# Performance work log

Hardware: AMD Instinct MI355X
Metric: run time of the kernel (lower is better)

The kernel has to match this reference:

```python
import jax, jax.numpy as jnp
import numpy as np

# dims
B = 4096; BEGIN = 0; END = 2048; N_OBJ = 64; D_OBJ = 32
PI_IN = 31; PI_H = 256; EMB = 256; H = 4; HD = 64; OTH_IN = 256; OTH_H = 256; OTH_OUT = 256

def _lin_init(k, fan_in, fan_out):
    b = np.sqrt(6.0 / (fan_in + fan_out))
    return jax.random.uniform(k, (fan_in, fan_out), jnp.float32, -b, b)

def setup_inputs() -> dict:
    key = jax.random.key(0)
    ks = jax.random.split(key, 8)
    obs = jax.random.normal(ks[0], (B, BEGIN + (END - BEGIN) + OTH_IN), jnp.float32)
    inp = {
        "obs": obs,
        # others encoder MLP: 256 -> 256 -> 256
        "oW1": _lin_init(ks[1], OTH_IN, OTH_H), "ob1": jnp.zeros((OTH_H,), jnp.float32),
        "oW2": _lin_init(ks[2], OTH_H, OTH_OUT), "ob2": jnp.zeros((OTH_OUT,), jnp.float32),
        # per-object pi MLP: 31 -> 256 -> 256 -> 256
        "pW1": _lin_init(ks[3], PI_IN, PI_H), "pb1": jnp.zeros((PI_H,), jnp.float32),
        "pW2": _lin_init(ks[4], PI_H, PI_H), "pb2": jnp.zeros((PI_H,), jnp.float32),
        "pW3": _lin_init(ks[5], PI_H, EMB), "pb3": jnp.zeros((EMB,), jnp.float32),
        # attention projections
        "Wq": _lin_init(ks[6], OTH_OUT, H * HD), "bq": jnp.zeros((H * HD,), jnp.float32),
        # per-head K/V projections (MultiHeadProj): [H, HD, HD], stored as x @ W per head
        "Wk": jax.random.uniform(jax.random.fold_in(key, 10), (H, HD, HD), jnp.float32, -np.sqrt(6.0/(2*HD)), np.sqrt(6.0/(2*HD))),
        "bk": jnp.zeros((H, HD), jnp.float32),
        "Wv": jax.random.uniform(jax.random.fold_in(key, 11), (H, HD, HD), jnp.float32, -np.sqrt(6.0/(2*HD)), np.sqrt(6.0/(2*HD))),
        "bv": jnp.zeros((H, HD), jnp.float32),
    }
    return inp

def reference(obs, oW1, ob1, oW2, ob2, pW1, pb1, pW2, pb2, pW3, pb3, Wq, bq, Wk, bk, Wv, bv):
    # split obs
    objs = obs[:, BEGIN:END].reshape(-1, N_OBJ, D_OBJ)
    others = jnp.concatenate([obs[:, :BEGIN], obs[:, END:]], axis=1)
    # others encoder
    others_e = jax.nn.relu(others @ oW1 + ob1) @ oW2 + ob2           # [B, 256]
    # mask + per-object MLP
    mask = objs[:, :, -1]                                            # [B, N]
    feats = objs[:, :, :-1]                                          # [B, N, 31]
    h = jax.nn.relu(feats @ pW1 + pb1)
    h = jax.nn.relu(h @ pW2 + pb2)
    emb = (h @ pW3 + pb3) * mask[:, :, None]                         # [B, N, EMB]
    # attention
    q = (others_e @ Wq + bq).reshape(-1, H, 1, HD)                   # [B, H, 1, HD]
    e = emb.reshape(-1, N_OBJ, H, HD)                                # [B, N, H, HD]
    key = jnp.einsum('bnhd,hde->bnhe', e, Wk) + bk                   # per-head linear
    val = (jnp.einsum('bnhd,hde->bnhe', e, Wv) + bv) * mask[:, :, None, None]
    logits = jnp.einsum('bhqd,bnhd->bhqn', q, key) / np.sqrt(EMB)    # [B, H, 1, N]
    logits = jnp.where(mask[:, None, None, :] == 0, -1e9, logits)
    attn = jax.nn.softmax(logits, axis=-1)
    out_emb = jnp.einsum('bhqn,bnhd->bhqd', attn, val).reshape(-1, EMB)
    return jnp.concatenate([others_e, out_emb], axis=1)             # [B, 512]
```

## Files before the change

### kernel.cpp

```cpp
#include <hip/hip_runtime.h>

#define BATCH      4096
#define OBS_COLS   2304
#define OTH_OFF    2048
#define EMB        256
#define OUTC       512

#define QK_BYTES   (4096u * 256u * 4u)
#define QB_BYTES   (4096u * 4u * 4u)

typedef __bf16 bf16x8 __attribute__((ext_vector_type(8)));
typedef __bf16 bf16x4 __attribute__((ext_vector_type(4)));
typedef float  f32x16 __attribute__((ext_vector_type(16)));

#define S_PW1  0
#define S_PW2  2
#define S_PW3  18
#define N_SLICE 34

__device__ __forceinline__ int shx(int row, int col) {
    return (row << 8) + ((((col >> 3) ^ (row & 31)) << 3) | (col & 7));
}

__global__ __launch_bounds__(512, 2) void k_oth(
    const float* __restrict__ obs,
    const float* __restrict__ oW1, const float* __restrict__ ob1,
    const float* __restrict__ oW2, const float* __restrict__ ob2,
    const float* __restrict__ Wq,  const float* __restrict__ bq,
    const float* __restrict__ Wk,  const float* __restrict__ bk,
    const float* __restrict__ pW1, const float* __restrict__ pW2,
    const float* __restrict__ pW3,
    float* __restrict__ out, float* __restrict__ qkg,
    float* __restrict__ qbg, __bf16* __restrict__ wp)
{
    __shared__ __align__(16) __bf16 s_a[32 * 256];
    __shared__ __align__(16) __bf16 s_h[32 * 256];
    __shared__ __align__(16) __bf16 s_q[32 * 256];
    __shared__ float s_qb[32 * 4];

    const int t  = threadIdx.x;
    const int b0 = blockIdx.x * 32;
    const int wv = t >> 6, lane = t & 63;
    const int lm = lane & 31, lh = lane >> 5;
    const int ct = wv;

    if (blockIdx.x < N_SLICE) {
        const int s = blockIdx.x;
        int kt; const float* W; int isW1 = 0;
        if      (s < S_PW2) { kt = s;         W = pW1; isW1 = 1; }
        else if (s < S_PW3) { kt = s - S_PW2; W = pW2; }
        else                { kt = s - S_PW3; W = pW3; }
        const int kbase = kt * 16 + lh * 8;
        const int n     = (t >> 6) * 32 + lm;
        bf16x8 v;
        #pragma unroll
        for (int j = 0; j < 8; ++j) {
            const int k = kbase + j;
            const float f = (isW1 && k >= 31) ? 0.0f : W[k * 256 + n];
            v[j] = (__bf16)f;
        }
        ((bf16x8*)wp)[(size_t)s * 512 + t] = v;
    }

    #pragma unroll
    for (int i = 0; i < 2; ++i) {
        const int c = i * 512 + t;
        const int row = c >> 5, seg = c & 31;
        const float* src = obs + (size_t)(b0 + row) * OBS_COLS + OTH_OFF + seg * 8;
        const float4 v0 = ((const float4*)src)[0];
        const float4 v1 = ((const float4*)src)[1];
        bf16x8 o;
        o[0]=(__bf16)v0.x; o[1]=(__bf16)v0.y; o[2]=(__bf16)v0.z; o[3]=(__bf16)v0.w;
        o[4]=(__bf16)v1.x; o[5]=(__bf16)v1.y; o[6]=(__bf16)v1.z; o[7]=(__bf16)v1.w;
        *(bf16x8*)&s_a[shx(row, seg * 8)] = o;
    }
    if (t < 128) s_qb[t] = 0.0f;
    __syncthreads();

    f32x16 acc;
    f32x16 vzero;
    #pragma unroll
    for (int i = 0; i < 16; ++i) vzero[i] = 0.0f;

    {
        const float* Wl = oW1 + (size_t)(lh * 8) * 256 + ct * 32 + lm;
        acc = vzero;
        float f[8];
        #pragma unroll
        for (int j = 0; j < 8; ++j) f[j] = Wl[j * 256];
        #pragma unroll 4
        for (int kt = 0; kt < 16; ++kt) {
            float fn[8];
            const int kn = (kt + 1) & 15;
            #pragma unroll
            for (int j = 0; j < 8; ++j) fn[j] = Wl[(kn * 16 + j) * 256];
            bf16x8 b;
            #pragma unroll
            for (int j = 0; j < 8; ++j) b[j] = (__bf16)f[j];
            const bf16x8 a = *(const bf16x8*)&s_a[shx(lm, kt * 16 + lh * 8)];
            acc = __builtin_amdgcn_mfma_f32_32x32x16_bf16(b, a, acc, 0, 0, 0);
            #pragma unroll
            for (int j = 0; j < 8; ++j) f[j] = fn[j];
        }
        const float* bias = &ob1[ct * 32 + 4 * lh];
        #pragma unroll
        for (int g = 0; g < 4; ++g) {
            bf16x4 v;
            #pragma unroll
            for (int q = 0; q < 4; ++q)
                v[q] = (__bf16)fmaxf(acc[g * 4 + q] + bias[8 * g + q], 0.0f);
            *(bf16x4*)&s_h[(lm << 8) + ((((ct << 2) + g) ^ lm) << 3) + 4 * lh] = v;
        }
    }
    __syncthreads();

    {
        const float* Wl = oW2 + (size_t)(lh * 8) * 256 + ct * 32 + lm;
        acc = vzero;
        float f[8];
        #pragma unroll
        for (int j = 0; j < 8; ++j) f[j] = Wl[j * 256];
        #pragma unroll 4
        for (int kt = 0; kt < 16; ++kt) {
            float fn[8];
            const int kn = (kt + 1) & 15;
            #pragma unroll
            for (int j = 0; j < 8; ++j) fn[j] = Wl[(kn * 16 + j) * 256];
            bf16x8 b;
            #pragma unroll
            for (int j = 0; j < 8; ++j) b[j] = (__bf16)f[j];
            const bf16x8 a = *(const bf16x8*)&s_h[shx(lm, kt * 16 + lh * 8)];
            acc = __builtin_amdgcn_mfma_f32_32x32x16_bf16(b, a, acc, 0, 0, 0);
            #pragma unroll
            for (int j = 0; j < 8; ++j) f[j] = fn[j];
        }
        const float* bias = &ob2[ct * 32 + 4 * lh];
        float* dstg = &out[(size_t)(b0 + lm) * OUTC + ct * 32 + 4 * lh];
        #pragma unroll
        for (int g = 0; g < 4; ++g) {
            float4 fv; bf16x4 v;
            float* fp = &fv.x;
            #pragma unroll
            for (int q = 0; q < 4; ++q) {
                const float f2 = acc[g * 4 + q] + bias[8 * g + q];
                fp[q] = f2; v[q] = (__bf16)f2;
            }
            *(float4*)&dstg[8 * g] = fv;
            *(bf16x4*)&s_a[(lm << 8) + ((((ct << 2) + g) ^ lm) << 3) + 4 * lh] = v;
        }
    }
    __syncthreads();

    {
        const float* Wl = Wq + (size_t)(lh * 8) * 256 + ct * 32 + lm;
        acc = vzero;
        float f[8];
        #pragma unroll
        for (int j = 0; j < 8; ++j) f[j] = Wl[j * 256];
        #pragma unroll 4
        for (int kt = 0; kt < 16; ++kt) {
            float fn[8];
            const int kn = (kt + 1) & 15;
            #pragma unroll
            for (int j = 0; j < 8; ++j) fn[j] = Wl[(kn * 16 + j) * 256];
            bf16x8 b;
            #pragma unroll
            for (int j = 0; j < 8; ++j) b[j] = (__bf16)f[j];
            const bf16x8 a = *(const bf16x8*)&s_a[shx(lm, kt * 16 + lh * 8)];
            acc = __builtin_amdgcn_mfma_f32_32x32x16_bf16(b, a, acc, 0, 0, 0);
            #pragma unroll
            for (int j = 0; j < 8; ++j) f[j] = fn[j];
        }
        const int hh = ct >> 1;
        const float* bias = &bq[ct * 32 + 4 * lh];
        const float* bkp  = &bk[ct * 32 + 4 * lh];
        float part = 0.0f;
        #pragma unroll
        for (int g = 0; g < 4; ++g) {
            bf16x4 v;
            #pragma unroll
            for (int q = 0; q < 4; ++q) {
                const float f2 = acc[g * 4 + q] + bias[8 * g + q];
                part += f2 * bkp[8 * g + q];
                v[q] = (__bf16)f2;
            }
            *(bf16x4*)&s_q[(lm << 8) + ((((ct << 2) + g) ^ lm) << 3) + 4 * lh] = v;
        }
        part += __shfl_xor(part, 32, 64);
        if (lane < 32) atomicAdd(&s_qb[lm * 4 + hh], part);
    }
    __syncthreads();

    if (t < 128) qbg[(size_t)(b0 + (t >> 2)) * 4 + (t & 3)] = s_qb[t];

    {
        const int h = wv >> 1, c2 = wv & 1;
        acc = vzero;
        #pragma unroll
        for (int kt = 0; kt < 4; ++kt) {
            const float* wk = Wk + ((size_t)(h * 64 + c2 * 32 + lm) * 64 + kt * 16 + lh * 8);
            const float4 w0 = *(const float4*)wk;
            const float4 w1 = *(const float4*)(wk + 4);
            bf16x8 b;
            b[0]=(__bf16)w0.x; b[1]=(__bf16)w0.y; b[2]=(__bf16)w0.z; b[3]=(__bf16)w0.w;
            b[4]=(__bf16)w1.x; b[5]=(__bf16)w1.y; b[6]=(__bf16)w1.z; b[7]=(__bf16)w1.w;
            const bf16x8 a = *(const bf16x8*)&s_q[shx(lm, h * 64 + kt * 16 + lh * 8)];
            acc = __builtin_amdgcn_mfma_f32_32x32x16_bf16(b, a, acc, 0, 0, 0);
        }
        float* dstg = &qkg[(size_t)(b0 + lm) * 256 + h * 64 + c2 * 32 + 4 * lh];
        #pragma unroll
        for (int g = 0; g < 4; ++g) {
            float4 fv;
            float* fp = &fv.x;
            #pragma unroll
            for (int q = 0; q < 4; ++q) fp[q] = acc[g * 4 + q];
            *(float4*)&dstg[8 * g] = fv;
        }
    }
}

__global__ __launch_bounds__(512, 4) void k_obj(
    const float* __restrict__ obs,  const __bf16* __restrict__ wp,
    const float* __restrict__ pb1,  const float* __restrict__ pb2,
    const float* __restrict__ pb3,  const float* __restrict__ qkg,
    const float* __restrict__ qbg,  const float* __restrict__ bv,
    const float* __restrict__ Wv,   float* __restrict__ out)
{
    __shared__ __align__(16) __bf16 s_h[128 * 256];
    __shared__ __align__(16) char s_fp[128 * 40 * 2];
    __bf16* s_f = (__bf16*)s_fp;
    float*  s_p = (float*)s_fp;
    __shared__ float s_mask[128];
    __shared__ float s_qk[8 * 64];
    __shared__ float s_am[8 * 64];
    __shared__ float s_amsum[8];

    const int t  = threadIdx.x;
    const int b0 = blockIdx.x * 2;
    const int wv = t >> 6, lane = t & 63;
    const int lm = lane & 31, lh = lane >> 5;
    const int rtp = wv & 1;
    const int ct0 = (wv >> 1) * 2;
    const int row0 = rtp * 64 + lm;
    const int row1 = row0 + 32;

    bf16x8 b1[2][2];
    {
        const bf16x8* Bg = (const bf16x8*)wp + S_PW1 * 512;
        #pragma unroll
        for (int kt = 0; kt < 2; ++kt)
            #pragma unroll
            for (int c = 0; c < 2; ++c)
                b1[kt][c] = Bg[(kt * 8 + ct0 + c) * 64 + lane];
    }

    {
        const int row = t >> 2, q4 = t & 3;
        const float* src = obs + (size_t)(b0 + (row >> 6)) * OBS_COLS
                               + (row & 63) * 32 + q4 * 8;
        const float4 v0 = ((const float4*)src)[0];
        const float4 v1 = ((const float4*)src)[1];
        bf16x8 o;
        o[0]=(__bf16)v0.x; o[1]=(__bf16)v0.y; o[2]=(__bf16)v0.z; o[3]=(__bf16)v0.w;
        o[4]=(__bf16)v1.x; o[5]=(__bf16)v1.y; o[6]=(__bf16)v1.z; o[7]=(__bf16)v1.w;
        *(bf16x8*)&s_f[row * 40 + q4 * 8] = o;
        if (q4 == 3) s_mask[row] = v1.w;
    }
    if (t < 128) ((float4*)s_qk)[t] = ((const float4*)(qkg + (size_t)b0 * 256))[t];
    __syncthreads();

    f32x16 acc[2][2];
    f32x16 vzero;
    #pragma unroll
    for (int i = 0; i < 16; ++i) vzero[i] = 0.0f;

    {
        #pragma unroll
        for (int r = 0; r < 2; ++r)
            #pragma unroll
            for (int c = 0; c < 2; ++c) acc[r][c] = vzero;
        #pragma unroll
        for (int kt = 0; kt < 2; ++kt) {
            const bf16x8 a0 = *(const bf16x8*)&s_f[row0 * 40 + kt * 16 + lh * 8];
            const bf16x8 a1 = *(const bf16x8*)&s_f[row1 * 40 + kt * 16 + lh * 8];
            acc[0][0] = __builtin_amdgcn_mfma_f32_32x32x16_bf16(b1[kt][0], a0, acc[0][0], 0, 0, 0);
            acc[0][1] = __builtin_amdgcn_mfma_f32_32x32x16_bf16(b1[kt][1], a0, acc[0][1], 0, 0, 0);
            acc[1][0] = __builtin_amdgcn_mfma_f32_32x32x16_bf16(b1[kt][0], a1, acc[1][0], 0, 0, 0);
            acc[1][1] = __builtin_amdgcn_mfma_f32_32x32x16_bf16(b1[kt][1], a1, acc[1][1], 0, 0, 0);
        }
        #pragma unroll
        for (int r = 0; r < 2; ++r) {
            const int row = r ? row1 : row0;
            #pragma unroll
            for (int c = 0; c < 2; ++c) {
                const float* bias = &pb1[(ct0 + c) * 32 + 4 * lh];
                #pragma unroll
                for (int g = 0; g < 4; ++g) {
                    bf16x4 v;
                    #pragma unroll
                    for (int q = 0; q < 4; ++q)
                        v[q] = (__bf16)fmaxf(acc[r][c][g * 4 + q] + bias[8 * g + q], 0.0f);
                    *(bf16x4*)&s_h[(row << 8) + (((((ct0 + c) << 2) + g) ^ lm) << 3) + 4 * lh] = v;
                }
            }
        }
    }
    __syncthreads();

    {
        const bf16x8* Bg = (const bf16x8*)wp + S_PW2 * 512;
        #pragma unroll
        for (int r = 0; r < 2; ++r)
            #pragma unroll
            for (int c = 0; c < 2; ++c) acc[r][c] = vzero;
        bf16x8 bc0 = Bg[(ct0 + 0) * 64 + lane];
        bf16x8 bc1 = Bg[(ct0 + 1) * 64 + lane];
        #pragma unroll 4
        for (int kt = 0; kt < 16; ++kt) {
            const int kn = (kt + 1) & 15;
            const bf16x8 bn0 = Bg[(kn * 8 + ct0 + 0) * 64 + lane];
            const bf16x8 bn1 = Bg[(kn * 8 + ct0 + 1) * 64 + lane];
            const bf16x8 a0 = *(const bf16x8*)&s_h[(row0 << 8) + (((2 * kt + lh) ^ lm) << 3)];
            const bf16x8 a1 = *(const bf16x8*)&s_h[(row1 << 8) + (((2 * kt + lh) ^ lm) << 3)];
            acc[0][0] = __builtin_amdgcn_mfma_f32_32x32x16_bf16(bc0, a0, acc[0][0], 0, 0, 0);
            acc[0][1] = __builtin_amdgcn_mfma_f32_32x32x16_bf16(bc1, a0, acc[0][1], 0, 0, 0);
            acc[1][0] = __builtin_amdgcn_mfma_f32_32x32x16_bf16(bc0, a1, acc[1][0], 0, 0, 0);
            acc[1][1] = __builtin_amdgcn_mfma_f32_32x32x16_bf16(bc1, a1, acc[1][1], 0, 0, 0);
            bc0 = bn0; bc1 = bn1;
        }
        __syncthreads();
        #pragma unroll
        for (int r = 0; r < 2; ++r) {
            const int row = r ? row1 : row0;
            #pragma unroll
            for (int c = 0; c < 2; ++c) {
                const float* bias = &pb2[(ct0 + c) * 32 + 4 * lh];
                #pragma unroll
                for (int g = 0; g < 4; ++g) {
                    bf16x4 v;
                    #pragma unroll
                    for (int q = 0; q < 4; ++q)
                        v[q] = (__bf16)fmaxf(acc[r][c][g * 4 + q] + bias[8 * g + q], 0.0f);
                    *(bf16x4*)&s_h[(row << 8) + (((((ct0 + c) << 2) + g) ^ lm) << 3) + 4 * lh] = v;
                }
            }
        }
    }
    __syncthreads();

    {
        const bf16x8* Bg = (const bf16x8*)wp + S_PW3 * 512;
        #pragma unroll
        for (int r = 0; r < 2; ++r)
            #pragma unroll
            for (int c = 0; c < 2; ++c) acc[r][c] = vzero;
        bf16x8 bc0 = Bg[(ct0 + 0) * 64 + lane];
        bf16x8 bc1 = Bg[(ct0 + 1) * 64 + lane];
        #pragma unroll 4
        for (int kt = 0; kt < 16; ++kt) {
            const int kn = (kt + 1) & 15;
            const bf16x8 bn0 = Bg[(kn * 8 + ct0 + 0) * 64 + lane];
            const bf16x8 bn1 = Bg[(kn * 8 + ct0 + 1) * 64 + lane];
            const bf16x8 a0 = *(const bf16x8*)&s_h[(row0 << 8) + (((2 * kt + lh) ^ lm) << 3)];
            const bf16x8 a1 = *(const bf16x8*)&s_h[(row1 << 8) + (((2 * kt + lh) ^ lm) << 3)];
            acc[0][0] = __builtin_amdgcn_mfma_f32_32x32x16_bf16(bc0, a0, acc[0][0], 0, 0, 0);
            acc[0][1] = __builtin_amdgcn_mfma_f32_32x32x16_bf16(bc1, a0, acc[0][1], 0, 0, 0);
            acc[1][0] = __builtin_amdgcn_mfma_f32_32x32x16_bf16(bc0, a1, acc[1][0], 0, 0, 0);
            acc[1][1] = __builtin_amdgcn_mfma_f32_32x32x16_bf16(bc1, a1, acc[1][1], 0, 0, 0);
            bc0 = bn0; bc1 = bn1;
        }
        __syncthreads();
        #pragma unroll
        for (int r = 0; r < 2; ++r) {
            const int row = r ? row1 : row0;
            const float mk = s_mask[row];
            #pragma unroll
            for (int c = 0; c < 2; ++c) {
                const float* bias = &pb3[(ct0 + c) * 32 + 4 * lh];
                #pragma unroll
                for (int g = 0; g < 4; ++g) {
                    bf16x4 v;
                    #pragma unroll
                    for (int q = 0; q < 4; ++q)
                        v[q] = (__bf16)((acc[r][c][g * 4 + q] + bias[8 * g + q]) * mk);
                    *(bf16x4*)&s_h[(row << 8) + (((((ct0 + c) << 2) + g) ^ lm) << 3) + 4 * lh] = v;
                }
            }
        }
    }
    __syncthreads();

    {
        const int r = wv >> 2, h = wv & 3;
        const float qb = qbg[(size_t)(b0 + r) * 4 + h];
        const int erow = r * 64 + lane;
        float dot = 0.0f;
        #pragma unroll
        for (int d8 = 0; d8 < 8; ++d8) {
            const bf16x8 ev = *(const bf16x8*)&s_h[(erow << 8) + ((((h << 3) + d8) ^ (erow & 31)) << 3)];
            const float* kv = &s_qk[(r * 4 + h) * 64 + d8 * 8];
            #pragma unroll
            for (int j = 0; j < 8; ++j) dot += (float)ev[j] * kv[j];
        }
        const float mk = s_mask[erow];
        float logit = (dot + qb) * 0.0625f;
        if (mk == 0.0f) logit = -1.0e9f;
        float m = logit;
        #pragma unroll
        for (int off = 32; off > 0; off >>= 1) m = fmaxf(m, __shfl_xor(m, off, 64));
        const float ex = __expf(logit - m);
        float ssum = ex;
        #pragma unroll
        for (int off = 32; off > 0; off >>= 1) ssum += __shfl_xor(ssum, off, 64);
        const float am = (ex / ssum) * mk;
        s_am[(r * 4 + h) * 64 + lane] = am;
        float ams = am;
        #pragma unroll
        for (int off = 32; off > 0; off >>= 1) ams += __shfl_xor(ams, off, 64);
        if (lane == 0) s_amsum[r * 4 + h] = ams;
    }
    __syncthreads();

    {
        const int r = t >> 8, h = (t >> 6) & 3, d = t & 63;
        const float* amr = &s_am[(r * 4 + h) * 64];
        const int blkbase = (h << 3) + (d >> 3);
        const int doff = d & 7;
        float a = 0.0f;
        #pragma unroll 16
        for (int n = 0; n < 64; ++n) {
            const int row = r * 64 + n;
            a += amr[n] * (float)s_h[(row << 8) + (((blkbase ^ (row & 31)) << 3) | doff)];
        }
        s_p[(r * 4 + h) * 64 + d] = a;
    }
    __syncthreads();

    {
        const int r = t >> 8, h = (t >> 6) & 3, e = t & 63;
        float a = s_amsum[r * 4 + h] * bv[h * 64 + e];
        const float* pr  = &s_p[(r * 4 + h) * 64];
        const float* wvp = Wv + (size_t)h * 64 * 64 + e;
        #pragma unroll 16
        for (int d = 0; d < 64; ++d)
            a += pr[d] * wvp[d * 64];
        out[(size_t)(b0 + r) * OUTC + EMB + h * 64 + e] = a;
    }
}

extern "C" void kernel_launch(void* const* d_in, const int* in_sizes, int n_in,
                              void* d_out, int out_size, void* d_ws, size_t ws_size,
                              hipStream_t stream)
{
    const float* obs = (const float*)d_in[0];
    const float* oW1 = (const float*)d_in[1];
    const float* ob1 = (const float*)d_in[2];
    const float* oW2 = (const float*)d_in[3];
    const float* ob2 = (const float*)d_in[4];
    const float* pW1 = (const float*)d_in[5];
    const float* pb1 = (const float*)d_in[6];
    const float* pW2 = (const float*)d_in[7];
    const float* pb2 = (const float*)d_in[8];
    const float* pW3 = (const float*)d_in[9];
    const float* pb3 = (const float*)d_in[10];
    const float* Wq  = (const float*)d_in[11];
    const float* bq  = (const float*)d_in[12];
    const float* Wk  = (const float*)d_in[13];
    const float* bk  = (const float*)d_in[14];
    const float* Wv  = (const float*)d_in[15];
    const float* bv  = (const float*)d_in[16];
    float*  out = (float*)d_out;
    float*  qkg = (float*)d_ws;
    float*  qbg = (float*)((char*)d_ws + QK_BYTES);
    __bf16* wp  = (__bf16*)((char*)d_ws + QK_BYTES + QB_BYTES);

    k_oth<<<BATCH / 32, 512, 0, stream>>>(obs, oW1, ob1, oW2, ob2, Wq, bq,
                                          Wk, bk, pW1, pW2, pW3,
                                          out, qkg, qbg, wp);
    k_obj<<<BATCH / 2, 512, 0, stream>>>(obs, wp, pb1, pb2, pb3, qkg, qbg,
                                         bv, Wv, out);
}
```

Measured before the change: 229.6 us.

## Process one batch row per block and vectorize attention epilogue with shuffle reductions

After: 240.7 us. +4.8%, slower.

```diff
diff --git a/kernel.cpp b/kernel.cpp
--- a/kernel.cpp
+++ b/kernel.cpp
@@ -219,30 +219,30 @@
     }
 }
 
-__global__ __launch_bounds__(512, 4) void k_obj(
+__global__ __launch_bounds__(256, 4) void k_obj(
     const float* __restrict__ obs,  const __bf16* __restrict__ wp,
     const float* __restrict__ pb1,  const float* __restrict__ pb2,
     const float* __restrict__ pb3,  const float* __restrict__ qkg,
     const float* __restrict__ qbg,  const float* __restrict__ bv,
     const float* __restrict__ Wv,   float* __restrict__ out)
 {
-    __shared__ __align__(16) __bf16 s_h[128 * 256];
-    __shared__ __align__(16) char s_fp[128 * 40 * 2];
+    __shared__ __align__(16) __bf16 s_h[64 * 256];
+    __shared__ __align__(16) char s_fp[64 * 32 * 2];
     __bf16* s_f = (__bf16*)s_fp;
     float*  s_p = (float*)s_fp;
-    __shared__ float s_mask[128];
-    __shared__ float s_qk[8 * 64];
-    __shared__ float s_am[8 * 64];
-    __shared__ float s_amsum[8];
+    __shared__ float s_mask[64];
+    __shared__ float s_qk[4 * 64];
+    __shared__ float s_am[4 * 64];
+    __shared__ float s_amsum[4];
+    __shared__ float s_qb[4];
 
     const int t  = threadIdx.x;
-    const int b0 = blockIdx.x * 2;
+    const int b  = blockIdx.x;
     const int wv = t >> 6, lane = t & 63;
     const int lm = lane & 31, lh = lane >> 5;
-    const int rtp = wv & 1;
-    const int ct0 = (wv >> 1) * 2;
-    const int row0 = rtp * 64 + lm;
-    const int row1 = row0 + 32;
+    const int ct0 = wv * 2;
+    const int row0 = lm;
+    const int row1 = lm + 32;
 
     bf16x8 b1[2][2];
     {
@@ -256,17 +256,17 @@
 
     {
         const int row = t >> 2, q4 = t & 3;
-        const float* src = obs + (size_t)(b0 + (row >> 6)) * OBS_COLS
-                               + (row & 63) * 32 + q4 * 8;
+        const float* src = obs + (size_t)b * OBS_COLS + row * 32 + q4 * 8;
         const float4 v0 = ((const float4*)src)[0];
         const float4 v1 = ((const float4*)src)[1];
         bf16x8 o;
         o[0]=(__bf16)v0.x; o[1]=(__bf16)v0.y; o[2]=(__bf16)v0.z; o[3]=(__bf16)v0.w;
         o[4]=(__bf16)v1.x; o[5]=(__bf16)v1.y; o[6]=(__bf16)v1.z; o[7]=(__bf16)v1.w;
-        *(bf16x8*)&s_f[row * 40 + q4 * 8] = o;
+        *(bf16x8*)&s_f[row * 32 + q4 * 8] = o;
         if (q4 == 3) s_mask[row] = v1.w;
     }
-    if (t < 128) ((float4*)s_qk)[t] = ((const float4*)(qkg + (size_t)b0 * 256))[t];
+    if (t < 64) ((float4*)s_qk)[t] = ((const float4*)(qkg + (size_t)b * 256))[t];
+    if (t >= 64 && t < 68) s_qb[t - 64] = qbg[(size_t)b * 4 + (t - 64)];
     __syncthreads();
 
     f32x16 acc[2][2];
@@ -281,8 +281,8 @@
             for (int c = 0; c < 2; ++c) acc[r][c] = vzero;
         #pragma unroll
         for (int kt = 0; kt < 2; ++kt) {
-            const bf16x8 a0 = *(const bf16x8*)&s_f[row0 * 40 + kt * 16 + lh * 8];
-            const bf16x8 a1 = *(const bf16x8*)&s_f[row1 * 40 + kt * 16 + lh * 8];
+            const bf16x8 a0 = *(const bf16x8*)&s_f[row0 * 32 + kt * 16 + lh * 8];
+            const bf16x8 a1 = *(const bf16x8*)&s_f[row1 * 32 + kt * 16 + lh * 8];
             acc[0][0] = __builtin_amdgcn_mfma_f32_32x32x16_bf16(b1[kt][0], a0, acc[0][0], 0, 0, 0);
             acc[0][1] = __builtin_amdgcn_mfma_f32_32x32x16_bf16(b1[kt][1], a0, acc[0][1], 0, 0, 0);
             acc[1][0] = __builtin_amdgcn_mfma_f32_32x32x16_bf16(b1[kt][0], a1, acc[1][0], 0, 0, 0);
@@ -391,18 +391,17 @@
     __syncthreads();
 
     {
-        const int r = wv >> 2, h = wv & 3;
-        const float qb = qbg[(size_t)(b0 + r) * 4 + h];
-        const int erow = r * 64 + lane;
+        const int h = wv;
+        const float qb = s_qb[h];
         float dot = 0.0f;
         #pragma unroll
         for (int d8 = 0; d8 < 8; ++d8) {
-            const bf16x8 ev = *(const bf16x8*)&s_h[(erow << 8) + ((((h << 3) + d8) ^ (erow & 31)) << 3)];
-            const float* kv = &s_qk[(r * 4 + h) * 64 + d8 * 8];
+            const bf16x8 ev = *(const bf16x8*)&s_h[(lane << 8) + ((((h << 3) + d8) ^ (lane & 31)) << 3)];
+            const float* kv = &s_qk[h * 64 + d8 * 8];
             #pragma unroll
             for (int j = 0; j < 8; ++j) dot += (float)ev[j] * kv[j];
         }
-        const float mk = s_mask[erow];
+        const float mk = s_mask[lane];
         float logit = (dot + qb) * 0.0625f;
         if (mk == 0.0f) logit = -1.0e9f;
         float m = logit;
@@ -413,38 +412,75 @@
         #pragma unroll
         for (int off = 32; off > 0; off >>= 1) ssum += __shfl_xor(ssum, off, 64);
         const float am = (ex / ssum) * mk;
-        s_am[(r * 4 + h) * 64 + lane] = am;
+        s_am[h * 64 + lane] = am;
         float ams = am;
         #pragma unroll
         for (int off = 32; off > 0; off >>= 1) ams += __shfl_xor(ams, off, 64);
-        if (lane == 0) s_amsum[r * 4 + h] = ams;
-    }
-    __syncthreads();
-
-    {
-        const int r = t >> 8, h = (t >> 6) & 3, d = t & 63;
-        const float* amr = &s_am[(r * 4 + h) * 64];
-        const int blkbase = (h << 3) + (d >> 3);
-        const int doff = d & 7;
-        float a = 0.0f;
-        #pragma unroll 16
-        for (int n = 0; n < 64; ++n) {
-            const int row = r * 64 + n;
-            a += amr[n] * (float)s_h[(row << 8) + (((blkbase ^ (row & 31)) << 3) | doff)];
-        }
-        s_p[(r * 4 + h) * 64 + d] = a;
-    }
-    __syncthreads();
-
-    {
-        const int r = t >> 8, h = (t >> 6) & 3, e = t & 63;
-        float a = s_amsum[r * 4 + h] * bv[h * 64 + e];
-        const float* pr  = &s_p[(r * 4 + h) * 64];
-        const float* wvp = Wv + (size_t)h * 64 * 64 + e;
-        #pragma unroll 16
-        for (int d = 0; d < 64; ++d)
-            a += pr[d] * wvp[d * 64];
-        out[(size_t)(b0 + r) * OUTC + EMB + h * 64 + e] = a;
+        if (lane == 0) s_amsum[h] = ams;
+    }
+    __syncthreads();
+
+    {
+        const int h = wv, dblk = lane >> 3, j = lane & 7;
+        const int blk = (h << 3) + dblk;
+        float a[8];
+        #pragma unroll
+        for (int dd = 0; dd < 8; ++dd) a[dd] = 0.0f;
+        #pragma unroll
+        for (int nn = 0; nn < 8; ++nn) {
+            const int n = j * 8 + nn;
+            const bf16x8 ev = *(const bf16x8*)&s_h[(n << 8) + ((blk ^ (n & 31)) << 3)];
+            const float amv = s_am[h * 64 + n];
+            #pragma unroll
+            for (int dd = 0; dd < 8; ++dd) a[dd] += amv * (float)ev[dd];
+        }
+        #pragma unroll
+        for (int off = 1; off <= 4; off <<= 1)
+            #pragma unroll
+            for (int dd = 0; dd < 8; ++dd) a[dd] += __shfl_xor(a[dd], off, 64);
+        const float s01 = (j & 1) ? a[1] : a[0];
+        const float s23 = (j & 1) ? a[3] : a[2];
+        const float s45 = (j & 1) ? a[5] : a[4];
+        const float s67 = (j & 1) ? a[7] : a[6];
+        const float t03 = (j & 2) ? s23 : s01;
+        const float t47 = (j & 2) ? s67 : s45;
+        const float val = (j & 4) ? t47 : t03;
+        s_p[h * 64 + dblk * 8 + j] = val;
+    }
+    __syncthreads();
+
+    {
+        const int h = wv, eblk = lane >> 3, j = lane & 7;
+        const float4 p0 = *(const float4*)&s_p[h * 64 + j * 8];
+        const float4 p1 = *(const float4*)&s_p[h * 64 + j * 8 + 4];
+        float pd[8] = {p0.x, p0.y, p0.z, p0.w, p1.x, p1.y, p1.z, p1.w};
+        float a[8];
+        #pragma unroll
+        for (int ee = 0; ee < 8; ++ee) a[ee] = 0.0f;
+        const float* wvb = Wv + (size_t)h * 4096 + eblk * 8;
+        #pragma unroll
+        for (int dd = 0; dd < 8; ++dd) {
+            const int d = j * 8 + dd;
+            const float4 w0 = *(const float4*)&wvb[d * 64];
+            const float4 w1 = *(const float4*)&wvb[d * 64 + 4];
+            a[0] += pd[dd] * w0.x; a[1] += pd[dd] * w0.y;
+            a[2] += pd[dd] * w0.z; a[3] += pd[dd] * w0.w;
+            a[4] += pd[dd] * w1.x; a[5] += pd[dd] * w1.y;
+            a[6] += pd[dd] * w1.z; a[7] += pd[dd] * w1.w;
+        }
+        #pragma unroll
+        for (int off = 1; off <= 4; off <<= 1)
+            #pragma unroll
+            for (int ee = 0; ee < 8; ++ee) a[ee] += __shfl_xor(a[ee], off, 64);
+        const float s01 = (j & 1) ? a[1] : a[0];
+        const float s23 = (j & 1) ? a[3] : a[2];
+        const float s45 = (j & 1) ? a[5] : a[4];
+        const float s67 = (j & 1) ? a[7] : a[6];
+        const float t03 = (j & 2) ? s23 : s01;
+        const float t47 = (j & 2) ? s67 : s45;
+        float val = (j & 4) ? t47 : t03;
+        val += s_amsum[h] * bv[h * 64 + lane];
+        out[(size_t)b * OUTC + EMB + h * 64 + lane] = val;
     }
 }
 
@@ -477,6 +513,6 @@
     k_oth<<<BATCH / 32, 512, 0, stream>>>(obs, oW1, ob1, oW2, ob2, Wq, bq,
                                           Wk, bk, pW1, pW2, pW3,
                                           out, qkg, qbg, wp);
-    k_obj<<<BATCH / 2, 512, 0, stream>>>(obs, wp, pb1, pb2, pb3, qkg, qbg,
-                                         bv, Wv, out);
+    k_obj<<<BATCH, 256, 0, stream>>>(obs, wp, pb1, pb2, pb3, qkg, qbg,
+                                     bv, Wv, out);
 }
```
